# Kernel optimization log

Hardware: AMD Instinct MI355X
Metric: run time of the kernel (lower is better)

Reference implementation:

```python
import jax, jax.numpy as jnp
import numpy as np

N_NODES = 100000
N_EDGES = 1600000
D = 128
N_LAYERS = 3


def _sage_layer(x, src, dst, Wl, Wr, bias, n_nodes):
    # mean aggregation of source-node features at destination nodes
    msg_sum = jax.ops.segment_sum(x[src], dst, num_segments=n_nodes)  # [N, D]
    cnt = jax.ops.segment_sum(jnp.ones((src.shape[0], 1), x.dtype), dst,
                              num_segments=n_nodes)  # [N, 1]
    mean = msg_sum / jnp.maximum(cnt, 1.0)
    # PyG SAGEConv: out = lin_l(aggr) + lin_r(x); lin_l carries the bias
    return mean @ Wl + x @ Wr + bias


def setup_inputs() -> dict:
    key = jax.random.key(0)
    k1, k2, k3, k4, k5 = jax.random.split(key, 5)
    scale = 1.0 / np.sqrt(D)
    x = jax.random.normal(k1, (N_NODES, D), dtype=jnp.float32)
    edge_index = jax.random.randint(k2, (2, N_EDGES), 0, N_NODES, dtype=jnp.int64)
    W_agg = jax.random.normal(k3, (N_LAYERS, D, D), dtype=jnp.float32) * scale
    W_root = jax.random.normal(k4, (N_LAYERS, D, D), dtype=jnp.float32) * scale
    b = jax.random.normal(k5, (N_LAYERS, D), dtype=jnp.float32) * scale
    return {"x": x, "edge_index": edge_index, "W_agg": W_agg,
            "W_root": W_root, "b": b}


def reference(x, edge_index, W_agg, W_root, b):
    src, dst = edge_index[0], edge_index[1]
    n = x.shape[0]
    # hidden layers: conv -> (dropout=identity in eval) -> relu
    for i in range(N_LAYERS - 1):
        x = _sage_layer(x, src, dst, W_agg[i], W_root[i], b[i], n)
        x = jax.nn.relu(x)
    # final layer: no relu
    x = _sage_layer(x, src, dst, W_agg[-1], W_root[-1], b[-1], n)
    return x
```

## Files before the change

kernel.cpp:

```cpp
#include <hip/hip_runtime.h>
#include <stdint.h>

#define D 128
#define CHUNK 6400

typedef __attribute__((ext_vector_type(8))) __bf16 bf16x8;
typedef __attribute__((ext_vector_type(4))) __bf16 bf16x4;
typedef __attribute__((ext_vector_type(4))) float f32x4;

__global__ void detect_idx(const void* ei, int* flag, int n_nodes) {
    if (blockIdx.x == 0 && threadIdx.x == 0) {
        const long long* p = (const long long*)ei;
        int is64 = 1;
        for (int i = 0; i < 64; ++i) {
            long long v = p[i];
            if (v < 0 || v >= (long long)n_nodes) { is64 = 0; break; }
        }
        *flag = is64;
    }
}

__global__ __launch_bounds__(256) void convert_pack(
        const void* __restrict__ ei, const int* __restrict__ flag,
        unsigned int* __restrict__ eword, unsigned char* __restrict__ gb,
        int* __restrict__ bcnt, int nE) {
    __shared__ int l[256];
    l[threadIdx.x] = 0;
    __syncthreads();
    bool is64 = *flag != 0;
    int stride = gridDim.x * 256;
    for (int e = blockIdx.x * 256 + threadIdx.x; e < nE; e += stride) {
        int s, d;
        if (is64) {
            const long long* p = (const long long*)ei;
            s = (int)p[e];
            d = (int)p[(size_t)nE + e];
        } else {
            const int* p = (const int*)ei;
            s = p[e];
            d = p[nE + e];
        }
        eword[e] = ((unsigned)s << 9) | (unsigned)(d & 511);
        gb[e] = (unsigned char)(d >> 9);
        atomicAdd(&l[d >> 9], 1);
    }
    __syncthreads();
    int v = l[threadIdx.x];
    if (v) atomicAdd(&bcnt[threadIdx.x], v);
}

__global__ void bucket_scan(const int* __restrict__ bcnt, int* __restrict__ bstart,
                            int* __restrict__ bcur, int G, int nE,
                            int* __restrict__ offsets, int n) {
    __shared__ int s[256];
    int t = threadIdx.x;
    int v = (t < G) ? bcnt[t] : 0;
    s[t] = v;
    __syncthreads();
    for (int off = 1; off < 256; off <<= 1) {
        int u = 0;
        if (t >= off) u = s[t - off];
        __syncthreads();
        if (t >= off) s[t] += u;
        __syncthreads();
    }
    if (t < G) { int ex = s[t] - v; bstart[t] = ex; bcur[t] = ex; }
    if (t == 0) offsets[n] = nE;
}

__global__ __launch_bounds__(256) void bucket_fill2(
        const unsigned int* __restrict__ eword, const unsigned char* __restrict__ gb,
        int* __restrict__ bcur, unsigned int* __restrict__ ebuf, int nE) {
    __shared__ unsigned int lw[CHUNK];
    __shared__ unsigned char lg[CHUNK];
    __shared__ int lcnt[256], lbase[256], lcur[256];
    int e0 = blockIdx.x * CHUNK;
    int cnt = nE - e0;
    if (cnt > CHUNK) cnt = CHUNK;
    if (cnt < 0) cnt = 0;
    for (int i = threadIdx.x; i < cnt; i += 256) {
        lw[i] = eword[e0 + i];
        lg[i] = gb[e0 + i];
    }
    lcnt[threadIdx.x] = 0;
    __syncthreads();
    for (int i = threadIdx.x; i < cnt; i += 256)
        atomicAdd(&lcnt[lg[i]], 1);
    __syncthreads();
    int c = lcnt[threadIdx.x];
    if (c > 0) lbase[threadIdx.x] = atomicAdd(&bcur[threadIdx.x], c);
    lcur[threadIdx.x] = 0;
    __syncthreads();
    for (int i = threadIdx.x; i < cnt; i += 256) {
        int g = lg[i];
        int p = lbase[g] + atomicAdd(&lcur[g], 1);
        ebuf[p] = lw[i];
    }
}

__global__ __launch_bounds__(256) void bucket_scatter2(
        const unsigned int* __restrict__ ebuf,
        const int* __restrict__ bstart, const int* __restrict__ bcnt,
        int* __restrict__ offsets, int* __restrict__ csr, int n) {
    __shared__ int ncnt[512], nofs[512], ps[256];
    int g = blockIdx.x;
    int base = bstart[g];
    int cnt = bcnt[g];
    int n0 = g << 9;
    int nr = n - n0; if (nr > 512) nr = 512;
    for (int i = threadIdx.x; i < 512; i += 256) ncnt[i] = 0;
    __syncthreads();
    for (int i = threadIdx.x; i < cnt; i += 256)
        atomicAdd(&ncnt[ebuf[base + i] & 511], 1);
    __syncthreads();
    int t = threadIdx.x;
    int c0 = ncnt[2 * t], c1 = ncnt[2 * t + 1];
    ps[t] = c0 + c1;
    __syncthreads();
    for (int off = 1; off < 256; off <<= 1) {
        int u = 0;
        if (t >= off) u = ps[t - off];
        __syncthreads();
        if (t >= off) ps[t] += u;
        __syncthreads();
    }
    int pex = ps[t] - (c0 + c1);
    nofs[2 * t] = pex;
    nofs[2 * t + 1] = pex + c0;
    __syncthreads();
    for (int i = threadIdx.x; i < nr; i += 256)
        offsets[n0 + i] = base + nofs[i];
    for (int i = threadIdx.x; i < 512; i += 256) ncnt[i] = 0;
    __syncthreads();
    for (int i = threadIdx.x; i < cnt; i += 256) {
        unsigned int w = ebuf[base + i];
        int d = w & 511;
        int p = base + nofs[d] + atomicAdd(&ncnt[d], 1);
        csr[p] = (int)(w >> 9);
    }
}

__global__ void build_wt(const float* __restrict__ Wa, const float* __restrict__ Wr,
                         __bf16* __restrict__ WtHi, __bf16* __restrict__ WtLo) {
    int idx = blockIdx.x * 256 + threadIdx.x;
    if (idx >= 3 * 128 * 256) return;
    int L = idx / (128 * 256);
    int rem = idx % (128 * 256);
    int c = rem / 256;
    int k = rem % 256;
    float v = (k < 128) ? Wa[((size_t)L * 128 + k) * 128 + c]
                        : Wr[((size_t)L * 128 + (k - 128)) * 128 + c];
    __bf16 h = (__bf16)v;
    __bf16 l = (__bf16)(v - (float)h);
    WtHi[idx] = h;
    WtLo[idx] = l;
}

__global__ void cvt_x(const float* __restrict__ x, __bf16* __restrict__ a,
                      int total8) {
    int i = blockIdx.x * 256 + threadIdx.x;
    if (i >= total8) return;
    const float4* p = (const float4*)(x + (size_t)i * 8);
    float4 v0 = p[0], v1 = p[1];
    float vv[8] = {v0.x, v0.y, v0.z, v0.w, v1.x, v1.y, v1.z, v1.w};
    bf16x8 h;
    #pragma unroll
    for (int j = 0; j < 8; ++j) h[j] = (__bf16)vv[j];
    *(bf16x8*)(a + (size_t)i * 8) = h;
}

__global__ __launch_bounds__(256) void agg_mean5(
        const __bf16* __restrict__ act, const int* __restrict__ csr,
        const int* __restrict__ offs, __bf16* __restrict__ mean, int n) {
    int node = (blockIdx.x * blockDim.x + threadIdx.x) >> 4;
    int l8 = (threadIdx.x & 15) << 3;
    if (node >= n) return;
    int beg = offs[node], end = offs[node + 1];
    float acc[8] = {0.f, 0.f, 0.f, 0.f, 0.f, 0.f, 0.f, 0.f};
    int i = beg;
    for (; i + 8 <= end; i += 8) {
        bf16x8 v[8];
        #pragma unroll
        for (int u = 0; u < 8; ++u)
            v[u] = *(const bf16x8*)(act + (size_t)csr[i + u] * D + l8);
        #pragma unroll
        for (int u = 0; u < 8; ++u)
            #pragma unroll
            for (int j = 0; j < 8; ++j) acc[j] += (float)v[u][j];
    }
    for (; i + 4 <= end; i += 4) {
        bf16x8 v[4];
        #pragma unroll
        for (int u = 0; u < 4; ++u)
            v[u] = *(const bf16x8*)(act + (size_t)csr[i + u] * D + l8);
        #pragma unroll
        for (int u = 0; u < 4; ++u)
            #pragma unroll
            for (int j = 0; j < 8; ++j) acc[j] += (float)v[u][j];
    }
    for (; i < end; ++i) {
        bf16x8 v = *(const bf16x8*)(act + (size_t)csr[i] * D + l8);
        #pragma unroll
        for (int j = 0; j < 8; ++j) acc[j] += (float)v[j];
    }
    int deg = end - beg;
    float inv = 1.0f / (float)(deg > 1 ? deg : 1);
    bf16x8 h;
    #pragma unroll
    for (int j = 0; j < 8; ++j) h[j] = (__bf16)(acc[j] * inv);
    *(bf16x8*)(mean + (size_t)node * D + l8) = h;
}

__global__ __launch_bounds__(512, 4) void sage_gemm8(
        const __bf16* __restrict__ mean, const __bf16* __restrict__ act,
        const __bf16* __restrict__ WtHi, const __bf16* __restrict__ WtLo,
        const float* __restrict__ bias,
        __bf16* __restrict__ oB, float* __restrict__ oF,
        int n, int mode, int npairs) {
    __shared__ __align__(16) char sA[2][2][8192];
    __shared__ __align__(16) char sC[2][8192];
    int tid  = threadIdx.x;
    int wave = tid >> 6;
    int lane = tid & 63;
    int r16  = lane & 15;
    int kg   = lane >> 4;
    int colbase = wave * 16;

    bf16x8 BH[8], BL[8];
    #pragma unroll
    for (int c8 = 0; c8 < 8; ++c8) {
        size_t o = (size_t)(colbase + r16) * 256 + c8 * 32 + kg * 8;
        BH[c8] = *(const bf16x8*)(WtHi + o);
        BL[c8] = *(const bf16x8*)(WtLo + o);
    }
    float4 bv = *(const float4*)(bias + colbase + kg * 4);

    int xm = (r16 & 7) << 4;
    int kb[8];
    #pragma unroll
    for (int c8 = 0; c8 < 8; ++c8)
        kb[c8] = r16 * 512 + ((c8 * 64 + kg * 16) ^ xm);

    int srow = tid >> 5;
    int sc16 = tid & 31;
    int sdst = srow * 512 + ((sc16 * 16) ^ ((srow & 7) << 4));

    auto stage_load = [&](int p, int half, int4& r) {
        int grow = p * 32 + half * 16 + srow;
        if (grow < n) {
            const __bf16* src = (sc16 < 16)
                ? (mean + (size_t)grow * D + sc16 * 8)
                : (act  + (size_t)grow * D + (sc16 - 16) * 8);
            r = *(const int4*)src;
        } else {
            r = make_int4(0, 0, 0, 0);
        }
    };

    int pstride = gridDim.x;
    int p = blockIdx.x;

    {
        int4 r0 = make_int4(0,0,0,0), r1 = make_int4(0,0,0,0);
        if (p < npairs) { stage_load(p, 0, r0); stage_load(p, 1, r1); }
        *(int4*)(sA[0][0] + sdst) = r0;
        *(int4*)(sA[0][1] + sdst) = r1;
    }
    __syncthreads();
    int cur = 0;

    for (; p < npairs; p += pstride) {
        int pn = p + pstride;
        bool hasnext = pn < npairs;
        int4 n0, n1;
        if (hasnext) { stage_load(pn, 0, n0); stage_load(pn, 1, n1); }

        f32x4 aH0 = (f32x4){0.f,0.f,0.f,0.f}, aL0 = aH0;
        f32x4 aH1 = aH0, aL1 = aH0;
        const char* b0 = sA[cur][0];
        const char* b1 = sA[cur][1];
        #pragma unroll
        for (int c8 = 0; c8 < 8; ++c8) {
            bf16x8 a0 = *(const bf16x8*)(b0 + kb[c8]);
            bf16x8 a1 = *(const bf16x8*)(b1 + kb[c8]);
            aH0 = __builtin_amdgcn_mfma_f32_16x16x32_bf16(BH[c8], a0, aH0, 0, 0, 0);
            aH1 = __builtin_amdgcn_mfma_f32_16x16x32_bf16(BH[c8], a1, aH1, 0, 0, 0);
            aL0 = __builtin_amdgcn_mfma_f32_16x16x32_bf16(BL[c8], a0, aL0, 0, 0, 0);
            aL1 = __builtin_amdgcn_mfma_f32_16x16x32_bf16(BL[c8], a1, aL1, 0, 0, 0);
        }

        __syncthreads();
        if (hasnext) {
            *(int4*)(sA[cur ^ 1][0] + sdst) = n0;
            *(int4*)(sA[cur ^ 1][1] + sdst) = n1;
        }

        #pragma unroll
        for (int h = 0; h < 2; ++h) {
            f32x4 a = h ? (aH1 + aL1) : (aH0 + aL0);
            float v0 = a[0] + bv.x;
            float v1 = a[1] + bv.y;
            float v2 = a[2] + bv.z;
            float v3 = a[3] + bv.w;
            if (mode == 0) {
                v0 = fmaxf(v0, 0.f); v1 = fmaxf(v1, 0.f);
                v2 = fmaxf(v2, 0.f); v3 = fmaxf(v3, 0.f);
                bf16x4 h4;
                h4[0] = (__bf16)v0; h4[1] = (__bf16)v1;
                h4[2] = (__bf16)v2; h4[3] = (__bf16)v3;
                *(bf16x4*)(sC[h] + r16 * 256 + (colbase + kg * 4) * 2) = h4;
            } else {
                *(f32x4*)(sC[h] + r16 * 512 + (colbase + kg * 4) * 4) =
                    (f32x4){v0, v1, v2, v3};
            }
        }
        __syncthreads();

        if (mode == 0) {
            int rr = tid >> 4, c16 = tid & 15;
            int grow = p * 32 + rr;
            if (grow < n) {
                int4 h = *(const int4*)(sC[rr >> 4] + (rr & 15) * 256 + c16 * 16);
                *(int4*)(oB + (size_t)grow * D + c16 * 8) = h;
            }
        } else {
            #pragma unroll
            for (int pass = 0; pass < 2; ++pass) {
                int chunk = pass * 512 + tid;
                int rr = chunk >> 5, c = chunk & 31;
                int grow = p * 32 + rr;
                if (grow < n) {
                    f32x4 f = *(const f32x4*)(sC[rr >> 4] + (rr & 15) * 512 + c * 16);
                    *(f32x4*)(oF + (size_t)grow * D + c * 4) = f;
                }
            }
        }
        cur ^= 1;
    }
}

extern "C" void kernel_launch(void* const* d_in, const int* in_sizes, int n_in,
                              void* d_out, int out_size, void* d_ws, size_t ws_size,
                              hipStream_t stream) {
    const float* x  = (const float*)d_in[0];
    const void*  ei = d_in[1];
    const float* Wa = (const float*)d_in[2];
    const float* Wr = (const float*)d_in[3];
    const float* bb = (const float*)d_in[4];
    float* outp = (float*)d_out;

    int n  = in_sizes[0] / D;
    int nE = in_sizes[1] / 2;
    int G  = (n + 511) >> 9;

    char* ws = (char*)d_ws;
    size_t off = 0;
    auto alloc = [&](size_t bytes) -> char* {
        char* p = ws + off;
        off = (off + bytes + 255) & ~(size_t)255;
        return p;
    };
    int* flag            = (int*)alloc(4);
    unsigned int* eword  = (unsigned int*)alloc((size_t)nE * 4);
    unsigned char* gbuf  = (unsigned char*)alloc((size_t)nE);
    unsigned int* ebuf   = (unsigned int*)alloc((size_t)nE * 4);
    int* offsets         = (int*)alloc(((size_t)n + 1) * 4);
    int* csr_src         = (int*)alloc((size_t)nE * 4);
    int* bcnt            = (int*)alloc(1024);
    int* bstart          = (int*)alloc(1024);
    int* bcur            = (int*)alloc(1024);
    __bf16* actA         = (__bf16*)alloc((size_t)n * D * 2);
    __bf16* actB         = (__bf16*)alloc((size_t)n * D * 2);
    __bf16* meanP        = (__bf16*)alloc((size_t)n * D * 2);
    __bf16* WtHi         = (__bf16*)alloc((size_t)3 * 128 * 256 * 2);
    __bf16* WtLo         = (__bf16*)alloc((size_t)3 * 128 * 256 * 2);
    (void)ws_size; (void)n_in; (void)out_size;

    const int B = 256;

    hipLaunchKernelGGL(detect_idx, dim3(1), dim3(64), 0, stream, ei, flag, n);
    hipMemsetAsync(bcnt, 0, 1024, stream);
    hipLaunchKernelGGL(convert_pack, dim3(512), dim3(B), 0, stream,
                       ei, flag, eword, gbuf, bcnt, nE);
    hipLaunchKernelGGL(build_wt, dim3(384), dim3(256), 0, stream, Wa, Wr, WtHi, WtLo);
    int total8 = n * D / 8;
    hipLaunchKernelGGL(cvt_x, dim3((total8 + 255) / 256), dim3(256), 0, stream,
                       x, actA, total8);

    hipLaunchKernelGGL(bucket_scan, dim3(1), dim3(B), 0, stream,
                       bcnt, bstart, bcur, G, nE, offsets, n);
    hipLaunchKernelGGL(bucket_fill2, dim3((nE + CHUNK - 1) / CHUNK), dim3(B), 0, stream,
                       eword, gbuf, bcur, ebuf, nE);
    hipLaunchKernelGGL(bucket_scatter2, dim3(G), dim3(B), 0, stream,
                       ebuf, bstart, bcnt, offsets, csr_src, n);

    int agg_blocks = (n * 16 + B - 1) / B;
    int npairs = (n + 31) / 32;
    int gemm_grid = 512;
    const int WSTRIDE = 128 * 256;

    hipLaunchKernelGGL(agg_mean5, dim3(agg_blocks), dim3(B), 0, stream,
                       actA, csr_src, offsets, meanP, n);
    hipLaunchKernelGGL(sage_gemm8, dim3(gemm_grid), dim3(512), 0, stream,
                       meanP, actA, WtHi + 0 * WSTRIDE, WtLo + 0 * WSTRIDE,
                       bb + 0 * D, actB, outp, n, 0, npairs);

    hipLaunchKernelGGL(agg_mean5, dim3(agg_blocks), dim3(B), 0, stream,
                       actB, csr_src, offsets, meanP, n);
    hipLaunchKernelGGL(sage_gemm8, dim3(gemm_grid), dim3(512), 0, stream,
                       meanP, actB, WtHi + 1 * WSTRIDE, WtLo + 1 * WSTRIDE,
                       bb + 1 * D, actA, outp, n, 0, npairs);

    hipLaunchKernelGGL(agg_mean5, dim3(agg_blocks), dim3(B), 0, stream,
                       actA, csr_src, offsets, meanP, n);
    hipLaunchKernelGGL(sage_gemm8, dim3(gemm_grid), dim3(512), 0, stream,
                       meanP, actA, WtHi + 2 * WSTRIDE, WtLo + 2 * WSTRIDE,
                       bb + 2 * D, actB, outp, n, 1, npairs);
}
```

Measured before the change: 329.4 us.

## Triple-buffer GEMM input staging with two-tile-ahead register prefetch

The GEMM kernel now keeps three shared-memory stages for the input tile and prefetches global loads two iterations ahead in registers. It writes the next-next stage before the MFMAs, which removes the barrier that sat between compute and the staging store. The full __syncthreads calls are replaced with an explicit lgkmcnt wait plus s_barrier, so global loads stay in flight across barriers. The cost is more LDS per block (three stages instead of two) and more live registers, which could lower occupancy. There is also a risk of races if the buffer rotation or barrier placement is wrong.

```diff
diff --git a/kernel.cpp b/kernel.cpp
--- a/kernel.cpp
+++ b/kernel.cpp
@@ -211,13 +211,13 @@
     *(bf16x8*)(mean + (size_t)node * D + l8) = h;
 }
 
-__global__ __launch_bounds__(512, 4) void sage_gemm8(
+__global__ __launch_bounds__(512, 4) void sage_gemm9(
         const __bf16* __restrict__ mean, const __bf16* __restrict__ act,
         const __bf16* __restrict__ WtHi, const __bf16* __restrict__ WtLo,
         const float* __restrict__ bias,
         __bf16* __restrict__ oB, float* __restrict__ oF,
         int n, int mode, int npairs) {
-    __shared__ __align__(16) char sA[2][2][8192];
+    __shared__ __align__(16) char sA[3][2][8192];
     __shared__ __align__(16) char sC[2][8192];
     int tid  = threadIdx.x;
     int wave = tid >> 6;
@@ -247,7 +247,7 @@
 
     auto stage_load = [&](int p, int half, int4& r) {
         int grow = p * 32 + half * 16 + srow;
-        if (grow < n) {
+        if (p < npairs && grow < n) {
             const __bf16* src = (sc16 < 16)
                 ? (mean + (size_t)grow * D + sc16 * 8)
                 : (act  + (size_t)grow * D + (sc16 - 16) * 8);
@@ -257,28 +257,41 @@
         }
     };
 
-    int pstride = gridDim.x;
-    int p = blockIdx.x;
+    int S  = gridDim.x;
+    int p0 = blockIdx.x;
 
     {
-        int4 r0 = make_int4(0,0,0,0), r1 = make_int4(0,0,0,0);
-        if (p < npairs) { stage_load(p, 0, r0); stage_load(p, 1, r1); }
-        *(int4*)(sA[0][0] + sdst) = r0;
-        *(int4*)(sA[0][1] + sdst) = r1;
-    }
-    __syncthreads();
-    int cur = 0;
-
-    for (; p < npairs; p += pstride) {
-        int pn = p + pstride;
-        bool hasnext = pn < npairs;
-        int4 n0, n1;
-        if (hasnext) { stage_load(pn, 0, n0); stage_load(pn, 1, n1); }
+        int4 a, b, c, d;
+        stage_load(p0, 0, a);     stage_load(p0, 1, b);
+        stage_load(p0 + S, 0, c); stage_load(p0 + S, 1, d);
+        *(int4*)(sA[0][0] + sdst) = a;
+        *(int4*)(sA[0][1] + sdst) = b;
+        *(int4*)(sA[1][0] + sdst) = c;
+        *(int4*)(sA[1][1] + sdst) = d;
+    }
+    __syncthreads();
+    int4 P0, P1;
+    stage_load(p0 + 2 * S, 0, P0);
+    stage_load(p0 + 2 * S, 1, P1);
+
+    int i = 0;
+    for (int p = p0; p < npairs; p += S, ++i) {
+        int bt  = i % 3;
+        int bt2 = (i + 2) % 3;
+
+        int4 Q0, Q1;
+        stage_load(p + 3 * S, 0, Q0);
+        stage_load(p + 3 * S, 1, Q1);
+
+        if (p + 2 * S < npairs) {
+            *(int4*)(sA[bt2][0] + sdst) = P0;
+            *(int4*)(sA[bt2][1] + sdst) = P1;
+        }
 
         f32x4 aH0 = (f32x4){0.f,0.f,0.f,0.f}, aL0 = aH0;
         f32x4 aH1 = aH0, aL1 = aH0;
-        const char* b0 = sA[cur][0];
-        const char* b1 = sA[cur][1];
+        const char* b0 = sA[bt][0];
+        const char* b1 = sA[bt][1];
         #pragma unroll
         for (int c8 = 0; c8 < 8; ++c8) {
             bf16x8 a0 = *(const bf16x8*)(b0 + kb[c8]);
@@ -287,12 +300,6 @@
             aH1 = __builtin_amdgcn_mfma_f32_16x16x32_bf16(BH[c8], a1, aH1, 0, 0, 0);
             aL0 = __builtin_amdgcn_mfma_f32_16x16x32_bf16(BL[c8], a0, aL0, 0, 0, 0);
             aL1 = __builtin_amdgcn_mfma_f32_16x16x32_bf16(BL[c8], a1, aL1, 0, 0, 0);
-        }
-
-        __syncthreads();
-        if (hasnext) {
-            *(int4*)(sA[cur ^ 1][0] + sdst) = n0;
-            *(int4*)(sA[cur ^ 1][1] + sdst) = n1;
         }
 
         #pragma unroll
@@ -314,7 +321,9 @@
                     (f32x4){v0, v1, v2, v3};
             }
         }
-        __syncthreads();
+
+        asm volatile("s_waitcnt lgkmcnt(0)" ::: "memory");
+        __builtin_amdgcn_s_barrier();
 
         if (mode == 0) {
             int rr = tid >> 4, c16 = tid & 15;
@@ -335,7 +344,11 @@
                 }
             }
         }
-        cur ^= 1;
+
+        asm volatile("s_waitcnt lgkmcnt(0)" ::: "memory");
+        __builtin_amdgcn_s_barrier();
+
+        P0 = Q0; P1 = Q1;
     }
 }
 
@@ -401,19 +414,19 @@
 
     hipLaunchKernelGGL(agg_mean5, dim3(agg_blocks), dim3(B), 0, stream,
                        actA, csr_src, offsets, meanP, n);
-    hipLaunchKernelGGL(sage_gemm8, dim3(gemm_grid), dim3(512), 0, stream,
+    hipLaunchKernelGGL(sage_gemm9, dim3(gemm_grid), dim3(512), 0, stream,
                        meanP, actA, WtHi + 0 * WSTRIDE, WtLo + 0 * WSTRIDE,
                        bb + 0 * D, actB, outp, n, 0, npairs);
 
     hipLaunchKernelGGL(agg_mean5, dim3(agg_blocks), dim3(B), 0, stream,
                        actB, csr_src, offsets, meanP, n);
-    hipLaunchKernelGGL(sage_gemm8, dim3(gemm_grid), dim3(512), 0, stream,
+    hipLaunchKernelGGL(sage_gemm9, dim3(gemm_grid), dim3(512), 0, stream,
                        meanP, actB, WtHi + 1 * WSTRIDE, WtLo + 1 * WSTRIDE,
                        bb + 1 * D, actA, outp, n, 0, npairs);
 
     hipLaunchKernelGGL(agg_mean5, dim3(agg_blocks), dim3(B), 0, stream,
                        actA, csr_src, offsets, meanP, n);
-    hipLaunchKernelGGL(sage_gemm8, dim3(gemm_grid), dim3(512), 0, stream,
+    hipLaunchKernelGGL(sage_gemm9, dim3(gemm_grid), dim3(512), 0, stream,
                        meanP, actA, WtHi + 2 * WSTRIDE, WtLo + 2 * WSTRIDE,
                        bb + 2 * D, actB, outp, n, 1, npairs);
 }
```

After: 333.2 us. No clear change (+1.2%).

## Quantize activations to per-row int8 before neighbor gather-aggregation

Applied to the files above, without the earlier changes.

Adds a per-layer pass that quantizes each bf16 activation row to unsigned 8-bit codes with a per-row float scale. The mean aggregation then gathers 8-byte int8 chunks plus one scale per neighbor instead of 16-byte bf16 chunks, halving gather traffic, and removes the 128 offset using the accumulated scale sum. This adds an extra kernel and a scale load per edge. It also introduces int8 quantization error into the aggregated means, which may break accuracy tolerance.

```diff
diff --git a/kernel.cpp b/kernel.cpp
--- a/kernel.cpp
+++ b/kernel.cpp
@@ -169,45 +169,118 @@
     *(bf16x8*)(a + (size_t)i * 8) = h;
 }
 
-__global__ __launch_bounds__(256) void agg_mean5(
-        const __bf16* __restrict__ act, const int* __restrict__ csr,
-        const int* __restrict__ offs, __bf16* __restrict__ mean, int n) {
+__global__ __launch_bounds__(256) void quant_act(
+        const __bf16* __restrict__ act, unsigned char* __restrict__ q,
+        float* __restrict__ scl, int n) {
+    int row = (blockIdx.x * blockDim.x + threadIdx.x) >> 4;
+    int l8 = (threadIdx.x & 15) << 3;
+    if (row >= n) return;
+    bf16x8 v = *(const bf16x8*)(act + (size_t)row * D + l8);
+    float f[8];
+    float m = 0.f;
+    #pragma unroll
+    for (int j = 0; j < 8; ++j) {
+        f[j] = (float)v[j];
+        m = fmaxf(m, fabsf(f[j]));
+    }
+    #pragma unroll
+    for (int off = 8; off >= 1; off >>= 1)
+        m = fmaxf(m, __shfl_xor(m, off));
+    float scale = m * (1.0f / 127.0f);
+    float inv = (m > 0.f) ? 127.0f / m : 0.f;
+    unsigned int a = 0, b = 0;
+    #pragma unroll
+    for (int j = 0; j < 4; ++j) {
+        unsigned int u = (unsigned int)(__float2int_rn(f[j] * inv) + 128);
+        a |= u << (8 * j);
+    }
+    #pragma unroll
+    for (int j = 0; j < 4; ++j) {
+        unsigned int u = (unsigned int)(__float2int_rn(f[4 + j] * inv) + 128);
+        b |= u << (8 * j);
+    }
+    *(int2*)(q + (size_t)row * D + l8) = make_int2((int)a, (int)b);
+    if ((threadIdx.x & 15) == 0) scl[row] = scale;
+}
+
+__global__ __launch_bounds__(256) void agg_mean6(
+        const unsigned char* __restrict__ q, const float* __restrict__ scl,
+        const int* __restrict__ csr, const int* __restrict__ offs,
+        __bf16* __restrict__ mean, int n) {
     int node = (blockIdx.x * blockDim.x + threadIdx.x) >> 4;
     int l8 = (threadIdx.x & 15) << 3;
     if (node >= n) return;
     int beg = offs[node], end = offs[node + 1];
     float acc[8] = {0.f, 0.f, 0.f, 0.f, 0.f, 0.f, 0.f, 0.f};
+    float S = 0.f;
     int i = beg;
     for (; i + 8 <= end; i += 8) {
-        bf16x8 v[8];
+        int2 v[8]; float s[8];
         #pragma unroll
-        for (int u = 0; u < 8; ++u)
-            v[u] = *(const bf16x8*)(act + (size_t)csr[i + u] * D + l8);
+        for (int u = 0; u < 8; ++u) {
+            int src = csr[i + u];
+            v[u] = *(const int2*)(q + (size_t)src * D + l8);
+            s[u] = scl[src];
+        }
         #pragma unroll
-        for (int u = 0; u < 8; ++u)
-            #pragma unroll
-            for (int j = 0; j < 8; ++j) acc[j] += (float)v[u][j];
+        for (int u = 0; u < 8; ++u) {
+            unsigned int a = (unsigned int)v[u].x, b = (unsigned int)v[u].y;
+            float sv = s[u];
+            S += sv;
+            acc[0] += (float)(a & 255u) * sv;
+            acc[1] += (float)((a >> 8) & 255u) * sv;
+            acc[2] += (float)((a >> 16) & 255u) * sv;
+            acc[3] += (float)(a >> 24) * sv;
+            acc[4] += (float)(b & 255u) * sv;
+            acc[5] += (float)((b >> 8) & 255u) * sv;
+            acc[6] += (float)((b >> 16) & 255u) * sv;
+            acc[7] += (float)(b >> 24) * sv;
+        }
     }
     for (; i + 4 <= end; i += 4) {
-        bf16x8 v[4];
+        int2 v[4]; float s[4];
         #pragma unroll
-        for (int u = 0; u < 4; ++u)
-            v[u] = *(const bf16x8*)(act + (size_t)csr[i + u] * D + l8);
+        for (int u = 0; u < 4; ++u) {
+            int src = csr[i + u];
+            v[u] = *(const int2*)(q + (size_t)src * D + l8);
+            s[u] = scl[src];
+        }
         #pragma unroll
-        for (int u = 0; u < 4; ++u)
-            #pragma unroll
-            for (int j = 0; j < 8; ++j) acc[j] += (float)v[u][j];
+        for (int u = 0; u < 4; ++u) {
+            unsigned int a = (unsigned int)v[u].x, b = (unsigned int)v[u].y;
+            float sv = s[u];
+            S += sv;
+            acc[0] += (float)(a & 255u) * sv;
+            acc[1] += (float)((a >> 8) & 255u) * sv;
+            acc[2] += (float)((a >> 16) & 255u) * sv;
+            acc[3] += (float)(a >> 24) * sv;
+            acc[4] += (float)(b & 255u) * sv;
+            acc[5] += (float)((b >> 8) & 255u) * sv;
+            acc[6] += (float)((b >> 16) & 255u) * sv;
+            acc[7] += (float)(b >> 24) * sv;
+        }
     }
     for (; i < end; ++i) {
-        bf16x8 v = *(const bf16x8*)(act + (size_t)csr[i] * D + l8);
-        #pragma unroll
-        for (int j = 0; j < 8; ++j) acc[j] += (float)v[j];
+        int src = csr[i];
+        int2 v = *(const int2*)(q + (size_t)src * D + l8);
+        float sv = scl[src];
+        unsigned int a = (unsigned int)v.x, b = (unsigned int)v.y;
+        S += sv;
+        acc[0] += (float)(a & 255u) * sv;
+        acc[1] += (float)((a >> 8) & 255u) * sv;
+        acc[2] += (float)((a >> 16) & 255u) * sv;
+        acc[3] += (float)(a >> 24) * sv;
+        acc[4] += (float)(b & 255u) * sv;
+        acc[5] += (float)((b >> 8) & 255u) * sv;
+        acc[6] += (float)((b >> 16) & 255u) * sv;
+        acc[7] += (float)(b >> 24) * sv;
     }
     int deg = end - beg;
     float inv = 1.0f / (float)(deg > 1 ? deg : 1);
     bf16x8 h;
     #pragma unroll
-    for (int j = 0; j < 8; ++j) h[j] = (__bf16)(acc[j] * inv);
+    for (int j = 0; j < 8; ++j)
+        h[j] = (__bf16)((acc[j] - 128.0f * S) * inv);
     *(bf16x8*)(mean + (size_t)node * D + l8) = h;
 }
 
@@ -372,6 +445,8 @@
     __bf16* actA         = (__bf16*)alloc((size_t)n * D * 2);
     __bf16* actB         = (__bf16*)alloc((size_t)n * D * 2);
     __bf16* meanP        = (__bf16*)alloc((size_t)n * D * 2);
+    unsigned char* qpl   = (unsigned char*)alloc((size_t)n * D);
+    float* scl           = (float*)alloc((size_t)n * 4);
     __bf16* WtHi         = (__bf16*)alloc((size_t)3 * 128 * 256 * 2);
     __bf16* WtLo         = (__bf16*)alloc((size_t)3 * 128 * 256 * 2);
     (void)ws_size; (void)n_in; (void)out_size;
@@ -394,25 +469,31 @@
     hipLaunchKernelGGL(bucket_scatter2, dim3(G), dim3(B), 0, stream,
                        ebuf, bstart, bcnt, offsets, csr_src, n);
 
-    int agg_blocks = (n * 16 + B - 1) / B;
+    int row_blocks = (n * 16 + B - 1) / B;
     int npairs = (n + 31) / 32;
     int gemm_grid = 512;
     const int WSTRIDE = 128 * 256;
 
-    hipLaunchKernelGGL(agg_mean5, dim3(agg_blocks), dim3(B), 0, stream,
-                       actA, csr_src, offsets, meanP, n);
+    hipLaunchKernelGGL(quant_act, dim3(row_blocks), dim3(B), 0, stream,
+                       actA, qpl, scl, n);
+    hipLaunchKernelGGL(agg_mean6, dim3(row_blocks), dim3(B), 0, stream,
+                       qpl, scl, csr_src, offsets, meanP, n);
     hipLaunchKernelGGL(sage_gemm8, dim3(gemm_grid), dim3(512), 0, stream,
                        meanP, actA, WtHi + 0 * WSTRIDE, WtLo + 0 * WSTRIDE,
                        bb + 0 * D, actB, outp, n, 0, npairs);
 
-    hipLaunchKernelGGL(agg_mean5, dim3(agg_blocks), dim3(B), 0, stream,
-                       actB, csr_src, offsets, meanP, n);
+    hipLaunchKernelGGL(quant_act, dim3(row_blocks), dim3(B), 0, stream,
+                       actB, qpl, scl, n);
+    hipLaunchKernelGGL(agg_mean6, dim3(row_blocks), dim3(B), 0, stream,
+                       qpl, scl, csr_src, offsets, meanP, n);
     hipLaunchKernelGGL(sage_gemm8, dim3(gemm_grid), dim3(512), 0, stream,
                        meanP, actB, WtHi + 1 * WSTRIDE, WtLo + 1 * WSTRIDE,
                        bb + 1 * D, actA, outp, n, 0, npairs);
 
-    hipLaunchKernelGGL(agg_mean5, dim3(agg_blocks), dim3(B), 0, stream,
-                       actA, csr_src, offsets, meanP, n);
+    hipLaunchKernelGGL(quant_act, dim3(row_blocks), dim3(B), 0, stream,
+                       actA, qpl, scl, n);
+    hipLaunchKernelGGL(agg_mean6, dim3(row_blocks), dim3(B), 0, stream,
+                       qpl, scl, csr_src, offsets, meanP, n);
     hipLaunchKernelGGL(sage_gemm8, dim3(gemm_grid), dim3(512), 0, stream,
                        meanP, actA, WtHi + 2 * WSTRIDE, WtLo + 2 * WSTRIDE,
                        bb + 2 * D, actB, outp, n, 1, npairs);
```

After: 311.1 us. -5.5%, faster.
